# Performance work log

Hardware: AMD Instinct MI355X
Metric: run time of the kernel (lower is better)

## Reference

```python
import jax, jax.numpy as jnp
import numpy as np

HID, HEADS, NL, WIN = 512, 4, 2, 5
DH = HID // HEADS
SLOPE = 0.2
EPS = 1e-5
B, L = 16, 1024
NEG_INF = -1e30


def _layer_norm(x, g, b):
    m = jnp.mean(x, axis=-1, keepdims=True)
    v = jnp.mean(jnp.square(x - m), axis=-1, keepdims=True)
    return (x - m) * jax.lax.rsqrt(v + EPS) * g + b


def _build_masks(attention_mask, last_starts, seq_len):
    # node layout: [g, h_1..h_T, l], total N = seq_len + 2
    bsz = attention_mask.shape[0]
    N = seq_len + 2
    pos = jnp.arange(N)
    last = last_starts[:, None, None]  # (B,1,1)
    global_mask = jnp.ones((bsz, 1, N), jnp.float32)
    # local node: g, itself, and tokens of the last utterance (node idx last+1 .. seq_len)
    local_mask = ((pos == 0) | (pos == N - 1) | ((pos >= last + 1) & (pos <= seq_len))).astype(jnp.float32)  # (B,1,N)
    # token nodes: global node + window of neighboring tokens
    ii = jnp.arange(seq_len)[:, None]          # query token index
    jj = jnp.arange(N)[None, :]                # key node index
    t = jj - 1                                 # token index of key node (valid in [0, seq_len))
    win = (t >= 0) & (t < seq_len) & (jnp.abs(ii - t) <= WIN)
    base = (jj == 0) | win                     # (L,N)
    # tokens at/after last utterance start also attend to the local node
    to_local = (jnp.arange(seq_len)[None, :, None] >= last_starts[:, None, None]) & (jj[None] == N - 1)  # (B,L,N)
    token_mask = (base[None] | to_local).astype(jnp.float32)
    # padding: key tokens masked by attention_mask; g and l always visible; padded queries fully masked
    ones_col = jnp.ones((bsz, seq_len, 1), jnp.float32)
    pad = jnp.concatenate([ones_col, jnp.broadcast_to(attention_mask[:, None, :], (bsz, seq_len, seq_len)), ones_col], axis=-1)
    token_mask = token_mask * pad * attention_mask[:, :, None]
    return global_mask, local_mask, token_mask


def _gat(q, kv, W, a, mask):
    # W: (hid, hid) as torch Linear weight (out,in); a: (H, 2*DH)
    bsz, Lq, _ = q.shape
    N = kv.shape[1]
    Q = (q @ W.T).reshape(bsz, Lq, HEADS, DH)
    K = (kv @ W.T).reshape(bsz, N, HEADS, DH)
    V = K  # key==value tensor in this module, same projection
    # additive score decomposes: (a . [Q||K]) = Q.a_q + K.a_k
    sq = jnp.einsum('bqhd,hd->bhq', Q, a[:, :DH])
    sk = jnp.einsum('bkhd,hd->bhk', K, a[:, DH:])
    s = sq[:, :, :, None] + sk[:, :, None, :]           # (B,H,Lq,N)
    s = jnp.where(s >= 0, s, SLOPE * s)                 # LeakyReLU
    s = jnp.where(mask[:, None, :, :] > 0, s, NEG_INF)
    w = jax.nn.softmax(s, axis=-1)
    w = jnp.where(jnp.isnan(w), 0.0, w)
    out = jnp.einsum('bhqk,bkhd->bqhd', w, V)
    return out.reshape(bsz, Lq, HID)


def setup_inputs() -> dict:
    key = jax.random.key(0)
    ks = jax.random.split(key, 10)
    scale = 1.0 / np.sqrt(HID)
    return {
        'global_embedding': jax.random.normal(ks[0], (B, HID), jnp.float32),
        'token_embeddings': jax.random.normal(ks[1], (B, L, HID), jnp.float32),
        'local_embedding': jax.random.normal(ks[2], (B, HID), jnp.float32),
        'attention_mask': jnp.ones((B, L), jnp.float32),
        'last_utterance_starts': jax.random.randint(ks[3], (B,), 0, 512, jnp.int32),
        'gat_W': jax.random.normal(ks[4], (NL, HID, HID), jnp.float32) * scale,
        'gat_a': jax.random.normal(ks[5], (NL, HEADS, 2 * DH), jnp.float32) * scale,
        'ln_gamma': jnp.ones((NL, HID), jnp.float32),
        'ln_beta': jnp.zeros((NL, HID), jnp.float32),
        'ffn_w1': jax.random.normal(ks[6], (3, HID, 4 * HID), jnp.float32) * scale,
        'ffn_b1': jnp.zeros((3, 4 * HID), jnp.float32),
        'ffn_w2': jax.random.normal(ks[7], (3, 4 * HID, HID), jnp.float32) * (1.0 / np.sqrt(4 * HID)),
        'ffn_b2': jnp.zeros((3, HID), jnp.float32),
        'out_ln_gamma': jnp.ones((3, HID), jnp.float32),
        'out_ln_beta': jnp.zeros((3, HID), jnp.float32),
    }


def reference(global_embedding, token_embeddings, local_embedding, attention_mask,
              last_utterance_starts, gat_W, gat_a, ln_gamma, ln_beta,
              ffn_w1, ffn_b1, ffn_w2, ffn_b2, out_ln_gamma, out_ln_beta):
    bsz, seq_len, _ = token_embeddings.shape
    gm, lm, tm = _build_masks(attention_mask, last_utterance_starts, seq_len)
    g = global_embedding[:, None, :]
    h = token_embeddings
    l = local_embedding[:, None, :]
    nodes = jnp.concatenate([g, h, l], axis=1)
    for k in range(NL):
        g_new = jax.nn.elu(_gat(g, nodes, gat_W[k], gat_a[k], gm))
        h_new = jax.nn.elu(_gat(h, nodes, gat_W[k], gat_a[k], tm))
        l_new = jax.nn.elu(_gat(l, nodes, gat_W[k], gat_a[k], lm))
        g = _layer_norm(g + g_new, ln_gamma[k], ln_beta[k])
        h = _layer_norm(h + h_new, ln_gamma[k], ln_beta[k])
        l = _layer_norm(l + l_new, ln_gamma[k], ln_beta[k])
        nodes = jnp.concatenate([g, h, l], axis=1)
    def ffn(x, i):
        hmid = jax.nn.gelu(x @ ffn_w1[i] + ffn_b1[i], approximate=False)
        return hmid @ ffn_w2[i] + ffn_b2[i]
    g = g + ffn(g, 0)
    h = h + ffn(h, 1)
    l = l + ffn(l, 2)
    updated_global = _layer_norm(g[:, 0], out_ln_gamma[0], out_ln_beta[0])
    updated_tokens = _layer_norm(h, out_ln_gamma[1], out_ln_beta[1])
    updated_local = _layer_norm(l[:, 0], out_ln_gamma[2], out_ln_beta[2])
    return updated_global, updated_tokens, updated_local
```

## Files before the change

### kernel.cpp

```cpp
#include <hip/hip_runtime.h>
#include <stdint.h>
#include <math.h>

#define HIDN 512
#define NHEAD 4
#define DHEAD 128
#define BATCH 16
#define SEQ 1024
#define NNODE 1026
#define MROWS (BATCH * NNODE)
#define MPAD 16512
#define MTOK (BATCH * SEQ)
#define FFD 2048
#define JCH 114

typedef short bf16x8 __attribute__((ext_vector_type(8)));
typedef float f32x4 __attribute__((ext_vector_type(4)));

__device__ __forceinline__ float bf2f(ushort u) {
    union { uint32_t i; float f; } v; v.i = ((uint32_t)u) << 16; return v.f;
}
__device__ __forceinline__ ushort f2bf(float f) {
    uint32_t x = __float_as_uint(f);
    return (ushort)((x + 0x7fffu + ((x >> 16) & 1u)) >> 16);
}
__device__ __forceinline__ float gelu(float v) {
    float z = v * 0.70710678118654752f;
    float az = fabsf(z);
    float t = __builtin_amdgcn_rcpf(1.f + 0.3275911f * az);
    float y = ((((1.061405429f * t - 1.453152027f) * t + 1.421413741f) * t
                - 0.284496736f) * t + 0.254829592f) * t;
    float e = __expf(-az * az);
    float erfv = 1.f - y * e;
    erfv = (z >= 0.f) ? erfv : -erfv;
    return 0.5f * v * (1.f + erfv);
}
__device__ __forceinline__ int cswz(int row, int col) {
    return row * 128 + ((((col >> 2) ^ (row & 7)) & 31) << 2) + (col & 3);
}

__global__ __launch_bounds__(256) void k_build_nodes(
    const float* __restrict__ g, const float* __restrict__ tok,
    const float* __restrict__ l, ushort* __restrict__ nb)
{
    int idx = blockIdx.x * 256 + threadIdx.x;
    int r = idx >> 9, c = idx & 511;
    float u = 0.f;
    if (r < MROWS) {
        int b = r / NNODE;
        int n = r - b * NNODE;
        if (n == 0)            u = g[b * HIDN + c];
        else if (n <= SEQ)     u = tok[((size_t)b * SEQ + (n - 1)) * HIDN + c];
        else                   u = l[b * HIDN + c];
    }
    nb[idx] = f2bf(u);
}

__global__ __launch_bounds__(256) void k_cvt(
    const float* __restrict__ in, ushort* __restrict__ out, int n)
{
    int idx = blockIdx.x * 256 + threadIdx.x;
    if (idx < n) out[idx] = f2bf(in[idx]);
}

__global__ __launch_bounds__(256) void k_transpose(
    const float* __restrict__ in, ushort* __restrict__ out, int R, int C)
{
    __shared__ float t[32][33];
    int x = blockIdx.x * 32 + threadIdx.x;
    int y0 = blockIdx.y * 32;
    for (int dy = threadIdx.y; dy < 32; dy += 8)
        t[dy][threadIdx.x] = in[(size_t)(y0 + dy) * C + x];
    __syncthreads();
    int ox = y0 + threadIdx.x;
    int oy0 = blockIdx.x * 32;
    for (int dy = threadIdx.y; dy < 32; dy += 8)
        out[(size_t)(oy0 + dy) * R + ox] = f2bf(t[threadIdx.x][dy]);
}

#define BM 128
#define BN 128
#define BK 64

__global__ __launch_bounds__(256) void k_gemm_bt(
    const ushort* __restrict__ A, const ushort* __restrict__ Bt,
    float* __restrict__ Cf, ushort* __restrict__ Cb,
    const float* __restrict__ bias,
    int N, int K, int ldb, int mode, int amap, int mguard, int first)
{
    __shared__ ushort smem[2 * (BM * BK + BN * BK)];
    int tid = threadIdx.x;
    int lane = tid & 63;
    int wave = tid >> 6;
    int wm = wave >> 1, wn = wave & 1;

    int GX = gridDim.x;
    int nwg = GX * gridDim.y;
    int bid = blockIdx.y * GX + blockIdx.x;
    int q = nwg >> 3, r = nwg & 7;
    int xcd = bid & 7, pos = bid >> 3;
    int cbase = (xcd < r) ? xcd * (q + 1) : r * (q + 1) + (xcd - r) * q;
    int wk = cbase + pos;
    int m0 = (wk / GX) * BM;
    int n0 = (wk % GX) * BN;

    f32x4 acc[4][4];
#pragma unroll
    for (int i = 0; i < 4; ++i)
#pragma unroll
        for (int j = 0; j < 4; ++j) acc[i][j] = (f32x4){0.f, 0.f, 0.f, 0.f};

    int lr = lane >> 3;
    int gco = ((lane & 7) ^ lr) * 8;

    const ushort* pA[4];
    const ushort* pB[4];
#pragma unroll
    for (int u = 0; u < 4; ++u) {
        int qq = wave * 4 + u;
        int rr8 = qq * 8 + lr;
        int grA = m0 + rr8;
        if (amap) grA = grA + 2 * (grA >> 10) + 1;
        pA[u] = A + (size_t)grA * K + gco;
        int grB = n0 + rr8;
        pB[u] = Bt + (size_t)grB * ldb + gco;
    }

    auto stage = [&](int buf) {
        ushort* sA = smem + buf * (BM * BK + BN * BK);
        ushort* sB = sA + BM * BK;
#pragma unroll
        for (int u = 0; u < 4; ++u) {
            int qq = wave * 4 + u;
            __builtin_amdgcn_global_load_lds(
                (const __attribute__((address_space(1))) void*)pA[u],
                (__attribute__((address_space(3))) void*)&sA[qq * 512], 16, 0, 0);
            __builtin_amdgcn_global_load_lds(
                (const __attribute__((address_space(1))) void*)pB[u],
                (__attribute__((address_space(3))) void*)&sB[qq * 512], 16, 0, 0);
            pA[u] += BK;
            pB[u] += BK;
        }
    };

    const int nk = K / BK;
    stage(0);
    __syncthreads();

    int rr = lane & 7;
    int rhi = (lane & 15) >> 3;
    for (int t = 0; t < nk; ++t) {
        if (t + 1 < nk) stage((t + 1) & 1);

        const ushort* sAr = smem + (t & 1) * (BM * BK + BN * BK);
        const ushort* sBr = sAr + BM * BK;
#pragma unroll
        for (int kk = 0; kk < BK; kk += 32) {
            int c4 = (kk >> 3) + (lane >> 4);
            int swz = rr * 64 + ((c4 ^ rr) << 3);
            bf16x8 af[4], bfr[4];
#pragma unroll
            for (int i = 0; i < 4; ++i)
                af[i] = *reinterpret_cast<const bf16x8*>(&sAr[(wm * 8 + i * 2 + rhi) * 512 + swz]);
#pragma unroll
            for (int j = 0; j < 4; ++j)
                bfr[j] = *reinterpret_cast<const bf16x8*>(&sBr[(wn * 8 + j * 2 + rhi) * 512 + swz]);
#pragma unroll
            for (int i = 0; i < 4; ++i)
#pragma unroll
                for (int j = 0; j < 4; ++j)
                    acc[i][j] = __builtin_amdgcn_mfma_f32_16x16x32_bf16(af[i], bfr[j], acc[i][j], 0, 0, 0);
        }
        asm volatile("s_waitcnt vmcnt(0)" ::: "memory");
        __builtin_amdgcn_s_barrier();
    }
    __syncthreads();

    float* sC = (float*)smem;
    int rb = (lane >> 4) * 4;
    int cb = lane & 15;
    int lrow = tid >> 2;
    int lcol = (tid & 3) << 5;
#pragma unroll
    for (int pass = 0; pass < 2; ++pass) {
        if (wm == pass) {
#pragma unroll
            for (int i = 0; i < 4; ++i)
#pragma unroll
                for (int j = 0; j < 4; ++j)
#pragma unroll
                    for (int rg = 0; rg < 4; ++rg)
                        sC[cswz(i * 16 + rb + rg, wn * 64 + j * 16 + cb)] = acc[i][j][rg];
        }
        __syncthreads();
        int gm = m0 + pass * 64 + lrow;
        if (gm < mguard) {
            int gn0 = n0 + lcol;
            float v[32];
#pragma unroll
            for (int e4 = 0; e4 < 8; ++e4) {
                float4 t = *(const float4*)&sC[cswz(lrow, lcol + e4 * 4)];
                v[e4 * 4 + 0] = t.x; v[e4 * 4 + 1] = t.y;
                v[e4 * 4 + 2] = t.z; v[e4 * 4 + 3] = t.w;
            }
            if (mode == 1 || mode == 3) {
                if (mode == 3) {
                    const float* a1 = bias + (gn0 >> 7) * 256 + (gn0 & 127);
                    const float* a2 = a1 + 128;
                    float s1 = 0.f, s2 = 0.f;
#pragma unroll
                    for (int j = 0; j < 32; ++j) {
                        s1 += v[j] * a1[j];
                        s2 += v[j] * a2[j];
                    }
                    s1 += __shfl_xor(s1, 1); s1 += __shfl_xor(s1, 2);
                    s2 += __shfl_xor(s2, 1); s2 += __shfl_xor(s2, 2);
                    if ((tid & 3) == 0) {
                        Cf[gm * 4 + (gn0 >> 7)] = s1;
                        Cf[(size_t)MPAD * 4 + gm * 4 + (gn0 >> 7)] = s2;
                    }
                }
                uint4* dst = (uint4*)(Cb + (size_t)gm * N + gn0);
#pragma unroll
                for (int q2 = 0; q2 < 4; ++q2) {
                    float s[8];
#pragma unroll
                    for (int t = 0; t < 8; ++t) {
                        float x = v[q2 * 8 + t];
                        s[t] = (mode == 1) ? gelu(x + bias[gn0 + q2 * 8 + t]) : x;
                    }
                    uint4 w;
                    w.x = (uint32_t)f2bf(s[0]) | ((uint32_t)f2bf(s[1]) << 16);
                    w.y = (uint32_t)f2bf(s[2]) | ((uint32_t)f2bf(s[3]) << 16);
                    w.z = (uint32_t)f2bf(s[4]) | ((uint32_t)f2bf(s[5]) << 16);
                    w.w = (uint32_t)f2bf(s[6]) | ((uint32_t)f2bf(s[7]) << 16);
                    dst[q2] = w;
                }
            } else {
                float4* dst = (float4*)(Cf + (size_t)gm * N + gn0);
#pragma unroll
                for (int e4 = 0; e4 < 8; ++e4) {
                    float4 t;
                    t.x = v[e4 * 4 + 0]; t.y = v[e4 * 4 + 1];
                    t.z = v[e4 * 4 + 2]; t.w = v[e4 * 4 + 3];
                    if (!first) {
                        float4 o = dst[e4];
                        t.x += o.x; t.y += o.y; t.z += o.z; t.w += o.w;
                    }
                    dst[e4] = t;
                }
            }
        }
        __syncthreads();
    }
}

#define QK 64

template<int NB>
__global__ __launch_bounds__(512) void k_g256(
    const ushort* __restrict__ A, const ushort* __restrict__ Bt,
    float* __restrict__ Cf, ushort* __restrict__ Cb,
    const float* __restrict__ bias,
    int N, int K, int mode, int amap)
{
    extern __shared__ ushort smem[];
    constexpr int FJ   = NB / 64;
    constexpr int BCH  = NB / 64;
    constexpr int BUFU = 16384 + NB * 64;
    constexpr int CW   = NB / 4;
    constexpr int CMSK = CW - 1;

    int tid = threadIdx.x;
    int lane = tid & 63;
    int wave = tid >> 6;
    int wr = wave >> 2;
    int wc = wave & 3;

    int GX = gridDim.x;
    int nwg = GX * gridDim.y;
    int bid = blockIdx.y * GX + blockIdx.x;
    int cpx = nwg >> 3;
    int wk = (bid & 7) * cpx + (bid >> 3);
    int m0 = (wk / GX) * 256;
    int n0 = (wk % GX) * NB;

    f32x4 acc[8][FJ];
#pragma unroll
    for (int i = 0; i < 8; ++i)
#pragma unroll
        for (int j = 0; j < FJ; ++j) acc[i][j] = (f32x4){0.f, 0.f, 0.f, 0.f};

    int lr = lane >> 3;
    int gco = ((lane & 7) ^ lr) * 8;

    const ushort* pA[4];
    const ushort* pB[BCH];
#pragma unroll
    for (int u = 0; u < 4; ++u) {
        int q = wave * 4 + u;
        int grA = m0 + q * 8 + lr;
        if (amap) grA = grA + 2 * (grA >> 10) + 1;
        pA[u] = A + (size_t)grA * K + gco;
    }
#pragma unroll
    for (int u = 0; u < BCH; ++u) {
        int q = wave * BCH + u;
        int grB = n0 + q * 8 + lr;
        pB[u] = Bt + (size_t)grB * K + gco;
    }

    auto stage = [&](int buf) {
        ushort* sA = smem + buf * BUFU;
        ushort* sB = sA + 16384;
#pragma unroll
        for (int u = 0; u < 4; ++u) {
            int q = wave * 4 + u;
            __builtin_amdgcn_global_load_lds(
                (const __attribute__((address_space(1))) void*)pA[u],
                (__attribute__((address_space(3))) void*)&sA[q * 512], 16, 0, 0);
            pA[u] += QK;
        }
#pragma unroll
        for (int u = 0; u < BCH; ++u) {
            int q = wave * BCH + u;
            __builtin_amdgcn_global_load_lds(
                (const __attribute__((address_space(1))) void*)pB[u],
                (__attribute__((address_space(3))) void*)&sB[q * 512], 16, 0, 0);
            pB[u] += QK;
        }
    };

    const int nk = K / QK;
    stage(0);
    __syncthreads();

    int rr = lane & 7;
    int rhi = (lane & 15) >> 3;
    for (int t = 0; t < nk; ++t) {
        if (t + 1 < nk) stage((t + 1) & 1);

        const ushort* sAr = smem + (t & 1) * BUFU;
        const ushort* sBr = sAr + 16384;
#pragma unroll
        for (int kk = 0; kk < 2; ++kk) {
            int c4 = kk * 4 + (lane >> 4);
            int swz = rr * 64 + ((c4 ^ rr) << 3);
#pragma unroll
            for (int fi0 = 0; fi0 < 8; fi0 += 4) {
                bf16x8 af[4];
#pragma unroll
                for (int i = 0; i < 4; ++i) {
                    int qA = wr * 16 + (fi0 + i) * 2 + rhi;
                    af[i] = *reinterpret_cast<const bf16x8*>(&sAr[qA * 512 + swz]);
                }
#pragma unroll
                for (int fj0 = 0; fj0 < FJ; fj0 += 2) {
                    bf16x8 bfr[2];
#pragma unroll
                    for (int j = 0; j < 2; ++j) {
                        int qB = wc * (NB / 32) + (fj0 + j) * 2 + rhi;
                        bfr[j] = *reinterpret_cast<const bf16x8*>(&sBr[qB * 512 + swz]);
                    }
#pragma unroll
                    for (int i = 0; i < 4; ++i)
#pragma unroll
                        for (int j = 0; j < 2; ++j)
                            acc[fi0 + i][fj0 + j] = __builtin_amdgcn_mfma_f32_16x16x32_bf16(
                                af[i], bfr[j], acc[fi0 + i][fj0 + j], 0, 0, 0);
                }
            }
        }
        __syncthreads();
    }

    float* sC = (float*)smem;
    int rb = (lane >> 4) * 4;
    int cb = lane & 15;
    int lrow = tid >> 2;
    int lcol = (tid & 3) * CW;
#pragma unroll
    for (int pass = 0; pass < 2; ++pass) {
        if (wr == pass) {
#pragma unroll
            for (int fi = 0; fi < 8; ++fi)
#pragma unroll
                for (int fj = 0; fj < FJ; ++fj)
#pragma unroll
                    for (int rg = 0; rg < 4; ++rg) {
                        int row = fi * 16 + rb + rg;
                        int col = wc * CW + fj * 16 + cb;
                        sC[row * NB + ((((col >> 2) ^ (row & 7)) & CMSK) << 2) + (col & 3)] =
                            acc[fi][fj][rg];
                    }
        }
        __syncthreads();
        int gm = m0 + pass * 128 + lrow;
        if (mode == 1) {
            uint4* dst = (uint4*)(Cb + (size_t)gm * N + n0 + lcol);
#pragma unroll
            for (int g = 0; g < CW / 8; ++g) {
                int col = lcol + g * 8;
                float4 a = *(const float4*)&sC[lrow * NB + ((((col >> 2) ^ (lrow & 7)) & CMSK) << 2)];
                float4 b = *(const float4*)&sC[lrow * NB + (((((col + 4) >> 2) ^ (lrow & 7)) & CMSK) << 2)];
                const float* bp = bias + n0 + col;
                float s0 = gelu(a.x + bp[0]), s1 = gelu(a.y + bp[1]);
                float s2 = gelu(a.z + bp[2]), s3 = gelu(a.w + bp[3]);
                float s4 = gelu(b.x + bp[4]), s5 = gelu(b.y + bp[5]);
                float s6 = gelu(b.z + bp[6]), s7 = gelu(b.w + bp[7]);
                uint4 w;
                w.x = (uint32_t)f2bf(s0) | ((uint32_t)f2bf(s1) << 16);
                w.y = (uint32_t)f2bf(s2) | ((uint32_t)f2bf(s3) << 16);
                w.z = (uint32_t)f2bf(s4) | ((uint32_t)f2bf(s5) << 16);
                w.w = (uint32_t)f2bf(s6) | ((uint32_t)f2bf(s7) << 16);
                dst[g] = w;
            }
        } else {
            float4* dst = (float4*)(Cf + (size_t)gm * N + n0 + lcol);
#pragma unroll
            for (int e4 = 0; e4 < CW / 4; ++e4) {
                int col = lcol + e4 * 4;
                float4 tv = *(const float4*)&sC[lrow * NB + ((((col >> 2) ^ (lrow & 7)) & CMSK) << 2)];
                dst[e4] = tv;
            }
        }
        __syncthreads();
    }
}

__global__ __launch_bounds__(256) void k_attn_token(
    const ushort* __restrict__ P, const float* __restrict__ sq, const float* __restrict__ sk,
    const float* __restrict__ am, const int* __restrict__ last,
    const float* __restrict__ gam, const float* __restrict__ bet,
    ushort* __restrict__ nb)
{
    int wid = blockIdx.x * 4 + (threadIdx.x >> 6);
    int tokid = ((wid & 7) << 11) | (wid >> 3);
    int b = tokid >> 10, i = tokid & 1023;
    int lane = threadIdx.x & 63;
    int hh = lane >> 4;
    int base = b * NNODE;
    int qrow = base + 1 + i;

    int kr[13];
    int val[13];
    int rowok = am[b * SEQ + i] > 0.f ? 1 : 0;
    kr[0] = base; val[0] = rowok;
#pragma unroll
    for (int s = 0; s < 11; ++s) {
        int t = i - 5 + s;
        int inb = (t >= 0) && (t <= SEQ - 1);
        int tt = inb ? t : 0;
        int v = inb && rowok && (am[b * SEQ + tt] > 0.f);
        kr[1 + s] = base + 1 + tt;
        val[1 + s] = v;
    }
    kr[12] = base + SEQ + 1;
    val[12] = (rowok && (i >= last[b])) ? 1 : 0;

    float sqv = sq[qrow * 4 + hh];
    float sc[13];
    float mx = -1e30f;
#pragma unroll
    for (int t = 0; t < 13; ++t) {
        float s = 0.f;
        if (val[t]) {
            s = sqv + sk[kr[t] * 4 + hh];
            s = s >= 0.f ? s : 0.2f * s;
            mx = fmaxf(mx, s);
        }
        sc[t] = s;
    }
    float den = 0.f;
#pragma unroll
    for (int t = 0; t < 13; ++t) {
        float ev = 0.f;
        if (val[t]) ev = expf(sc[t] - mx);
        sc[t] = ev; den += ev;
    }
    float inv = (den > 1e-30f && den < 1e30f) ? 1.f / den : 0.f;

    int o0 = lane * 8;
    float accv[8] = {0.f, 0.f, 0.f, 0.f, 0.f, 0.f, 0.f, 0.f};
#pragma unroll
    for (int t = 0; t < 13; ++t) {
        if (val[t]) {
            float wgt = sc[t] * inv;
            const ushort* pv = P + (size_t)kr[t] * HIDN + o0;
#pragma unroll
            for (int d = 0; d < 8; ++d) accv[d] += wgt * bf2f(pv[d]);
        }
    }

    ushort* nrow = nb + (size_t)qrow * HIDN + o0;
    float x[8], s1 = 0.f, s2 = 0.f;
#pragma unroll
    for (int d = 0; d < 8; ++d) {
        float v = accv[d];
        v = v > 0.f ? v : expf(v) - 1.f;
        v += bf2f(nrow[d]);
        x[d] = v; s1 += v; s2 += v * v;
    }
#pragma unroll
    for (int off = 32; off; off >>= 1) { s1 += __shfl_xor(s1, off); s2 += __shfl_xor(s2, off); }
    float mean = s1 * (1.f / 512.f);
    float var = s2 * (1.f / 512.f) - mean * mean; var = fmaxf(var, 0.f);
    float rn = rsqrtf(var + 1e-5f);
#pragma unroll
    for (int d = 0; d < 8; ++d) {
        float y = (x[d] - mean) * rn * gam[o0 + d] + bet[o0 + d];
        nrow[d] = f2bf(y);
    }
}

__global__ __launch_bounds__(256) void k_glsm(
    const float* __restrict__ sq, const float* __restrict__ sk,
    const int* __restrict__ last,
    float* __restrict__ ebuf, float* __restrict__ einv)
{
    __shared__ float red[1024];
    int rw = blockIdx.x, b = rw >> 1, isl = rw & 1;
    int base = b * NNODE;
    int qrow = base + (isl ? (SEQ + 1) : 0);
    int lastb = last[b];
    int tid = threadIdx.x;

    float sqh[4];
#pragma unroll
    for (int h = 0; h < 4; ++h) sqh[h] = sq[qrow * 4 + h];

    float mx[4] = {-1e30f, -1e30f, -1e30f, -1e30f};
    for (int j = tid; j < NNODE; j += 256) {
        bool ok = !isl || (j == 0 || j == SEQ + 1 || (j >= lastb + 1 && j <= SEQ));
        if (ok) {
#pragma unroll
            for (int h = 0; h < 4; ++h) {
                float s = sqh[h] + sk[(base + j) * 4 + h];
                s = s >= 0.f ? s : 0.2f * s;
                mx[h] = fmaxf(mx[h], s);
            }
        }
    }
#pragma unroll
    for (int h = 0; h < 4; ++h) red[tid * 4 + h] = mx[h];
    __syncthreads();
    for (int s = 128; s; s >>= 1) {
        if (tid < s) {
#pragma unroll
            for (int h = 0; h < 4; ++h)
                red[tid * 4 + h] = fmaxf(red[tid * 4 + h], red[(tid + s) * 4 + h]);
        }
        __syncthreads();
    }
#pragma unroll
    for (int h = 0; h < 4; ++h) mx[h] = red[h];
    __syncthreads();

    float sm[4] = {0.f, 0.f, 0.f, 0.f};
    for (int j = tid; j < NNODE; j += 256) {
        bool ok = !isl || (j == 0 || j == SEQ + 1 || (j >= lastb + 1 && j <= SEQ));
#pragma unroll
        for (int h = 0; h < 4; ++h) {
            float v = 0.f;
            if (ok) {
                float s = sqh[h] + sk[(base + j) * 4 + h];
                s = s >= 0.f ? s : 0.2f * s;
                v = expf(s - mx[h]);
            }
            ebuf[((size_t)rw * NNODE + j) * 4 + h] = v;
            sm[h] += v;
        }
    }
#pragma unroll
    for (int h = 0; h < 4; ++h) red[tid * 4 + h] = sm[h];
    __syncthreads();
    for (int s = 128; s; s >>= 1) {
        if (tid < s) {
#pragma unroll
            for (int h = 0; h < 4; ++h) red[tid * 4 + h] += red[(tid + s) * 4 + h];
        }
        __syncthreads();
    }
    if (tid < 4) {
        float den = red[tid];
        einv[rw * 4 + tid] = (den > 1e-30f && den < 1e30f) ? 1.f / den : 0.f;
    }
}

__global__ __launch_bounds__(256) void k_glpv(
    const ushort* __restrict__ P, const float* __restrict__ ebuf,
    float* __restrict__ pout2)
{
    __shared__ float es[JCH * 4];
    int p = blockIdx.x, rw = blockIdx.y;
    int b = rw >> 1;
    int base = b * NNODE;
    int tid = threadIdx.x;
    for (int t = tid; t < JCH * 4; t += 256)
        es[t] = ebuf[((size_t)rw * NNODE + p * JCH) * 4 + t];
    __syncthreads();
    int o0 = tid, o1 = tid + 256;
    int h0 = o0 >> 7, h1 = o1 >> 7;
    const ushort* Pb = P + (size_t)(base + p * JCH) * HIDN;
    float a0 = 0.f, a1 = 0.f;
    for (int j = 0; j < JCH; ++j) {
        const ushort* pr = Pb + (size_t)j * HIDN;
        a0 += es[j * 4 + h0] * bf2f(pr[o0]);
        a1 += es[j * 4 + h1] * bf2f(pr[o1]);
    }
    float* o = pout2 + ((size_t)rw * 9 + p) * HIDN;
    o[o0] = a0;
    o[o1] = a1;
}

__global__ __launch_bounds__(256) void k_glred(
    const float* __restrict__ pout2, const float* __restrict__ einv,
    const float* __restrict__ gam, const float* __restrict__ bet,
    ushort* __restrict__ nb)
{
    __shared__ float red[512];
    int rw = blockIdx.x, b = rw >> 1, isl = rw & 1;
    size_t qrow = (size_t)b * NNODE + (isl ? SEQ + 1 : 0);
    int tid = threadIdx.x;
    float xv[2], s1 = 0.f, s2 = 0.f;
#pragma unroll
    for (int u = 0; u < 2; ++u) {
        int o = tid + u * 256;
        int h = o >> 7;
        float acc = 0.f;
#pragma unroll
        for (int p = 0; p < 9; ++p)
            acc += pout2[((size_t)rw * 9 + p) * HIDN + o];
        acc *= einv[rw * 4 + h];
        float v = acc > 0.f ? acc : expf(acc) - 1.f;
        v += bf2f(nb[qrow * HIDN + o]);
        xv[u] = v; s1 += v; s2 += v * v;
    }
    red[tid] = s1;
    __syncthreads();
    for (int s = 128; s; s >>= 1) { if (tid < s) red[tid] += red[tid + s]; __syncthreads(); }
    float mean = red[0] * (1.f / 512.f);
    __syncthreads();
    red[tid] = s2;
    __syncthreads();
    for (int s = 128; s; s >>= 1) { if (tid < s) red[tid] += red[tid + s]; __syncthreads(); }
    float var = red[0] * (1.f / 512.f) - mean * mean; var = fmaxf(var, 0.f);
    float rn = rsqrtf(var + 1e-5f);
#pragma unroll
    for (int u = 0; u < 2; ++u) {
        int o = tid + u * 256;
        float y = (xv[u] - mean) * rn * gam[o] + bet[o];
        nb[qrow * HIDN + o] = f2bf(y);
    }
}

__global__ __launch_bounds__(256) void k_fgl1(
    const ushort* __restrict__ nb, const float* __restrict__ w1,
    float* __restrict__ pmid)
{
    __shared__ float xs[64];
    int p = blockIdx.x, rw = blockIdx.y;
    int b = rw >> 1, isl = rw & 1;
    int idx = isl ? 2 : 0;
    size_t nrow = (size_t)b * NNODE + (isl ? SEQ + 1 : 0);
    int tid = threadIdx.x;
    if (tid < 64) xs[tid] = bf2f(nb[nrow * HIDN + p * 64 + tid]);
    __syncthreads();
    const float* W1 = w1 + (size_t)idx * HIDN * FFD + (size_t)p * 64 * FFD;
    float acc[8] = {0.f, 0.f, 0.f, 0.f, 0.f, 0.f, 0.f, 0.f};
    for (int ii = 0; ii < 64; ++ii) {
        float xv = xs[ii];
        const float* wrow = W1 + (size_t)ii * FFD + tid;
#pragma unroll
        for (int u = 0; u < 8; ++u) acc[u] += xv * wrow[u * 256];
    }
    float* o = pmid + ((size_t)rw * 8 + p) * FFD + tid;
#pragma unroll
    for (int u = 0; u < 8; ++u) o[u * 256] = acc[u];
}

__global__ __launch_bounds__(256) void k_fgl2(
    const float* __restrict__ pmid, const float* __restrict__ b1,
    float* __restrict__ mid)
{
    int g = blockIdx.x * 256 + threadIdx.x;
    int e4 = g * 4;
    int rw = e4 >> 11;
    int m = e4 & 2047;
    int isl = rw & 1;
    int idx = isl ? 2 : 0;
#pragma unroll
    for (int d = 0; d < 4; ++d) {
        float s = 0.f;
#pragma unroll
        for (int p = 0; p < 8; ++p)
            s += pmid[((size_t)rw * 8 + p) * FFD + m + d];
        s += b1[idx * FFD + m + d];
        mid[(size_t)rw * FFD + m + d] = gelu(s);
    }
}

__global__ __launch_bounds__(256) void k_fgl3(
    const float* __restrict__ mid, const float* __restrict__ w2,
    float* __restrict__ pout)
{
    __shared__ float ms[256];
    int p = blockIdx.x, rw = blockIdx.y;
    int isl = rw & 1;
    int idx = isl ? 2 : 0;
    int tid = threadIdx.x;
    ms[tid] = mid[(size_t)rw * FFD + p * 256 + tid];
    __syncthreads();
    const float* W2 = w2 + (size_t)idx * FFD * HIDN + (size_t)p * 256 * HIDN;
    float a0 = 0.f, a1 = 0.f;
    for (int mm = 0; mm < 256; ++mm) {
        float mv = ms[mm];
        const float* wrow = W2 + (size_t)mm * HIDN + tid;
        a0 += mv * wrow[0];
        a1 += mv * wrow[256];
    }
    float* o = pout + ((size_t)rw * 8 + p) * HIDN + tid;
    o[0] = a0;
    o[256] = a1;
}

__global__ __launch_bounds__(256) void k_fgl4(
    const float* __restrict__ pout, const float* __restrict__ b2,
    const ushort* __restrict__ nb,
    const float* __restrict__ og, const float* __restrict__ obt,
    float* __restrict__ out)
{
    __shared__ float red[512];
    int rw = blockIdx.x;
    int b = rw >> 1, isl = rw & 1;
    int idx = isl ? 2 : 0;
    size_t nrow = (size_t)b * NNODE + (isl ? SEQ + 1 : 0);
    int tid = threadIdx.x;
    float xv[2], s1 = 0.f, s2 = 0.f;
#pragma unroll
    for (int u = 0; u < 2; ++u) {
        int o = tid + u * 256;
        float s = 0.f;
#pragma unroll
        for (int p = 0; p < 8; ++p)
            s += pout[((size_t)rw * 8 + p) * HIDN + o];
        s += b2[idx * HIDN + o] + bf2f(nb[nrow * HIDN + o]);
        xv[u] = s; s1 += s; s2 += s * s;
    }
    red[tid] = s1;
    __syncthreads();
    for (int s = 128; s; s >>= 1) { if (tid < s) red[tid] += red[tid + s]; __syncthreads(); }
    float mean = red[0] * (1.f / 512.f);
    __syncthreads();
    red[tid] = s2;
    __syncthreads();
    for (int s = 128; s; s >>= 1) { if (tid < s) red[tid] += red[tid + s]; __syncthreads(); }
    float var = red[0] * (1.f / 512.f) - mean * mean; var = fmaxf(var, 0.f);
    float rn = rsqrtf(var + 1e-5f);
    size_t obase = isl ? ((size_t)8192 + (size_t)MTOK * HIDN + (size_t)b * HIDN)
                       : ((size_t)b * HIDN);
#pragma unroll
    for (int u = 0; u < 2; ++u) {
        int o = tid + u * 256;
        out[obase + o] = (xv[u] - mean) * rn * og[idx * HIDN + o] + obt[idx * HIDN + o];
    }
}

__global__ __launch_bounds__(64) void k_ln_final(
    float* __restrict__ Pt, const ushort* __restrict__ nb,
    const float* __restrict__ b2,
    const float* __restrict__ gam, const float* __restrict__ bet)
{
    int r = blockIdx.x, lane = threadIdx.x;
    int nrow = r + 2 * (r >> 10) + 1;
    int o0 = lane * 8;
    float* x = Pt + (size_t)r * HIDN + o0;
    const ushort* res = nb + (size_t)nrow * HIDN + o0;
    float v[8], s1 = 0.f, s2 = 0.f;
#pragma unroll
    for (int d = 0; d < 8; ++d) {
        float t = x[d] + b2[o0 + d] + bf2f(res[d]);
        v[d] = t; s1 += t; s2 += t * t;
    }
#pragma unroll
    for (int off = 32; off; off >>= 1) { s1 += __shfl_xor(s1, off); s2 += __shfl_xor(s2, off); }
    float mean = s1 * (1.f / 512.f);
    float var = s2 * (1.f / 512.f) - mean * mean; var = fmaxf(var, 0.f);
    float rn = rsqrtf(var + 1e-5f);
#pragma unroll
    for (int d = 0; d < 8; ++d)
        x[d] = (v[d] - mean) * rn * gam[o0 + d] + bet[o0 + d];
}

extern "C" void kernel_launch(void* const* d_in, const int* in_sizes, int n_in,
                              void* d_out, int out_size, void* d_ws, size_t ws_size,
                              hipStream_t stream)
{
    (void)in_sizes; (void)n_in; (void)out_size; (void)ws_size;
    const float* g_emb   = (const float*)d_in[0];
    const float* tok_emb = (const float*)d_in[1];
    const float* l_emb   = (const float*)d_in[2];
    const float* am      = (const float*)d_in[3];
    const int*   last    = (const int*)d_in[4];
    const float* gat_W   = (const float*)d_in[5];
    const float* gat_a   = (const float*)d_in[6];
    const float* ln_g    = (const float*)d_in[7];
    const float* ln_b    = (const float*)d_in[8];
    const float* ffn_w1  = (const float*)d_in[9];
    const float* ffn_b1  = (const float*)d_in[10];
    const float* ffn_w2  = (const float*)d_in[11];
    const float* ffn_b2  = (const float*)d_in[12];
    const float* oln_g   = (const float*)d_in[13];
    const float* oln_b   = (const float*)d_in[14];
    float* out = (float*)d_out;

    char* w = (char*)d_ws;
    ushort* nodes_b = (ushort*)w; w += (size_t)MPAD * HIDN * 2;
    char*   scratch = w;          w += (size_t)8 * 1024 * 1024;
    ushort* w1t     = (ushort*)w; w += (size_t)FFD * HIDN * 2;
    ushort* w2t     = (ushort*)w; w += (size_t)FFD * HIDN * 2;
    ushort* gatWb   = (ushort*)w; w += (size_t)2 * HIDN * HIDN * 2;
    float*  sqb     = (float*)w;  w += (size_t)MPAD * 4 * 4;
    float*  skb     = (float*)w;  w += (size_t)MPAD * 4 * 4;
    ushort* Hmid    = (ushort*)w; w += (size_t)MTOK * FFD * 2;

    float* pmid = (float*)scratch;
    float* mid  = pmid + (size_t)32 * 8 * FFD;
    float* pout = mid + (size_t)32 * FFD;
    float* ebuf  = (float*)(scratch + (size_t)3 * 1024 * 1024);
    float* einv  = ebuf + (size_t)32 * NNODE * 4;
    float* pout2 = einv + 128;

    ushort* P = (ushort*)out;
    float* Pt = out + 8192;

    k_build_nodes<<<MPAD * HIDN / 256, 256, 0, stream>>>(g_emb, tok_emb, l_emb, nodes_b);
    k_cvt<<<(2 * HIDN * HIDN) / 256, 256, 0, stream>>>(gat_W, gatWb, 2 * HIDN * HIDN);
    k_transpose<<<dim3(FFD / 32, HIDN / 32), dim3(32, 8), 0, stream>>>(ffn_w1 + (size_t)HIDN * FFD, w1t, HIDN, FFD);
    k_transpose<<<dim3(HIDN / 32, FFD / 32), dim3(32, 8), 0, stream>>>(ffn_w2 + (size_t)FFD * HIDN, w2t, FFD, HIDN);

    for (int k = 0; k < 2; ++k) {
        k_gemm_bt<<<dim3(HIDN / BN, MPAD / BM), 256, 0, stream>>>(
            nodes_b, gatWb + (size_t)k * HIDN * HIDN, sqb, P,
            gat_a + k * NHEAD * 2 * DHEAD,
            HIDN, HIDN, HIDN, 3, 0, MROWS, 1);
        k_attn_token<<<MTOK / 4, 256, 0, stream>>>(P, sqb, skb, am, last,
                                                   ln_g + k * HIDN, ln_b + k * HIDN, nodes_b);
        k_glsm<<<32, 256, 0, stream>>>(sqb, skb, last, ebuf, einv);
        k_glpv<<<dim3(9, 32), 256, 0, stream>>>(P, ebuf, pout2);
        k_glred<<<32, 256, 0, stream>>>(pout2, einv, ln_g + k * HIDN, ln_b + k * HIDN, nodes_b);
    }

    k_fgl1<<<dim3(8, 32), 256, 0, stream>>>(nodes_b, ffn_w1, pmid);
    k_fgl2<<<64, 256, 0, stream>>>(pmid, ffn_b1, mid);
    k_fgl3<<<dim3(8, 32), 256, 0, stream>>>(mid, ffn_w2, pout);
    k_fgl4<<<32, 256, 0, stream>>>(pout, ffn_b2, nodes_b, oln_g, oln_b, out);

    k_g256<256><<<dim3(FFD / 256, MTOK / 256), 512, 131072, stream>>>(
        nodes_b, w1t, nullptr, Hmid, ffn_b1 + FFD, FFD, HIDN, 1, 1);
    k_g256<128><<<dim3(HIDN / 128, MTOK / 256), 512, 98304, stream>>>(
        Hmid, w2t, Pt, nullptr, nullptr, HIDN, FFD, 0, 0);
    k_ln_final<<<MTOK, 64, 0, stream>>>(Pt, nodes_b, ffn_b2 + HIDN, oln_g + HIDN, oln_b + HIDN);
}
```

Before: 477.6 us.

## Fuse global/local node attention softmax, PV and layernorm into one kernel

New measurement: 692.4 us. +45.0%, slower.

```diff
diff --git a/kernel.cpp b/kernel.cpp
--- a/kernel.cpp
+++ b/kernel.cpp
@@ -12,7 +12,6 @@
 #define MPAD 16512
 #define MTOK (BATCH * SEQ)
 #define FFD 2048
-#define JCH 114
 
 typedef short bf16x8 __attribute__((ext_vector_type(8)));
 typedef float f32x4 __attribute__((ext_vector_type(4)));
@@ -513,144 +512,116 @@
     }
 }
 
-__global__ __launch_bounds__(256) void k_glsm(
-    const float* __restrict__ sq, const float* __restrict__ sk,
-    const int* __restrict__ last,
-    float* __restrict__ ebuf, float* __restrict__ einv)
-{
-    __shared__ float red[1024];
+__global__ __launch_bounds__(1024) void k_glatt(
+    const ushort* __restrict__ P, const float* __restrict__ sq,
+    const float* __restrict__ sk, const int* __restrict__ last,
+    const float* __restrict__ gam, const float* __restrict__ bet,
+    ushort* __restrict__ nb)
+{
+    __shared__ float es[NNODE * 4];
+    __shared__ float red[64];
+    __shared__ float xv2[512];
     int rw = blockIdx.x, b = rw >> 1, isl = rw & 1;
     int base = b * NNODE;
-    int qrow = base + (isl ? (SEQ + 1) : 0);
+    size_t qrow = (size_t)base + (isl ? (SEQ + 1) : 0);
     int lastb = last[b];
     int tid = threadIdx.x;
+    int lane = tid & 63, wave = tid >> 6;
 
     float sqh[4];
 #pragma unroll
     for (int h = 0; h < 4; ++h) sqh[h] = sq[qrow * 4 + h];
 
     float mx[4] = {-1e30f, -1e30f, -1e30f, -1e30f};
-    for (int j = tid; j < NNODE; j += 256) {
+    for (int j = tid; j < NNODE; j += 1024) {
         bool ok = !isl || (j == 0 || j == SEQ + 1 || (j >= lastb + 1 && j <= SEQ));
-        if (ok) {
-#pragma unroll
-            for (int h = 0; h < 4; ++h) {
-                float s = sqh[h] + sk[(base + j) * 4 + h];
+#pragma unroll
+        for (int h = 0; h < 4; ++h) {
+            float s = -1e30f;
+            if (ok) {
+                s = sqh[h] + sk[(base + j) * 4 + h];
                 s = s >= 0.f ? s : 0.2f * s;
                 mx[h] = fmaxf(mx[h], s);
             }
-        }
-    }
-#pragma unroll
-    for (int h = 0; h < 4; ++h) red[tid * 4 + h] = mx[h];
-    __syncthreads();
-    for (int s = 128; s; s >>= 1) {
-        if (tid < s) {
-#pragma unroll
-            for (int h = 0; h < 4; ++h)
-                red[tid * 4 + h] = fmaxf(red[tid * 4 + h], red[(tid + s) * 4 + h]);
-        }
-        __syncthreads();
-    }
-#pragma unroll
-    for (int h = 0; h < 4; ++h) mx[h] = red[h];
+            es[j * 4 + h] = s;
+        }
+    }
+#pragma unroll
+    for (int off = 32; off; off >>= 1)
+#pragma unroll
+        for (int h = 0; h < 4; ++h) mx[h] = fmaxf(mx[h], __shfl_xor(mx[h], off));
+    if (lane == 0) {
+#pragma unroll
+        for (int h = 0; h < 4; ++h) red[wave * 4 + h] = mx[h];
+    }
+    __syncthreads();
+#pragma unroll
+    for (int h = 0; h < 4; ++h) {
+        float m = -1e30f;
+        for (int w2 = 0; w2 < 16; ++w2) m = fmaxf(m, red[w2 * 4 + h]);
+        mx[h] = m;
+    }
     __syncthreads();
 
     float sm[4] = {0.f, 0.f, 0.f, 0.f};
-    for (int j = tid; j < NNODE; j += 256) {
-        bool ok = !isl || (j == 0 || j == SEQ + 1 || (j >= lastb + 1 && j <= SEQ));
+    for (int j = tid; j < NNODE; j += 1024) {
 #pragma unroll
         for (int h = 0; h < 4; ++h) {
-            float v = 0.f;
-            if (ok) {
-                float s = sqh[h] + sk[(base + j) * 4 + h];
-                s = s >= 0.f ? s : 0.2f * s;
-                v = expf(s - mx[h]);
-            }
-            ebuf[((size_t)rw * NNODE + j) * 4 + h] = v;
-            sm[h] += v;
-        }
-    }
-#pragma unroll
-    for (int h = 0; h < 4; ++h) red[tid * 4 + h] = sm[h];
-    __syncthreads();
-    for (int s = 128; s; s >>= 1) {
-        if (tid < s) {
-#pragma unroll
-            for (int h = 0; h < 4; ++h) red[tid * 4 + h] += red[(tid + s) * 4 + h];
-        }
-        __syncthreads();
-    }
-    if (tid < 4) {
-        float den = red[tid];
-        einv[rw * 4 + tid] = (den > 1e-30f && den < 1e30f) ? 1.f / den : 0.f;
-    }
-}
-
-__global__ __launch_bounds__(256) void k_glpv(
-    const ushort* __restrict__ P, const float* __restrict__ ebuf,
-    float* __restrict__ pout2)
-{
-    __shared__ float es[JCH * 4];
-    int p = blockIdx.x, rw = blockIdx.y;
-    int b = rw >> 1;
-    int base = b * NNODE;
-    int tid = threadIdx.x;
-    for (int t = tid; t < JCH * 4; t += 256)
-        es[t] = ebuf[((size_t)rw * NNODE + p * JCH) * 4 + t];
-    __syncthreads();
-    int o0 = tid, o1 = tid + 256;
-    int h0 = o0 >> 7, h1 = o1 >> 7;
-    const ushort* Pb = P + (size_t)(base + p * JCH) * HIDN;
-    float a0 = 0.f, a1 = 0.f;
-    for (int j = 0; j < JCH; ++j) {
-        const ushort* pr = Pb + (size_t)j * HIDN;
-        a0 += es[j * 4 + h0] * bf2f(pr[o0]);
-        a1 += es[j * 4 + h1] * bf2f(pr[o1]);
-    }
-    float* o = pout2 + ((size_t)rw * 9 + p) * HIDN;
-    o[o0] = a0;
-    o[o1] = a1;
-}
-
-__global__ __launch_bounds__(256) void k_glred(
-    const float* __restrict__ pout2, const float* __restrict__ einv,
-    const float* __restrict__ gam, const float* __restrict__ bet,
-    ushort* __restrict__ nb)
-{
-    __shared__ float red[512];
-    int rw = blockIdx.x, b = rw >> 1, isl = rw & 1;
-    size_t qrow = (size_t)b * NNODE + (isl ? SEQ + 1 : 0);
-    int tid = threadIdx.x;
-    float xv[2], s1 = 0.f, s2 = 0.f;
-#pragma unroll
-    for (int u = 0; u < 2; ++u) {
-        int o = tid + u * 256;
-        int h = o >> 7;
-        float acc = 0.f;
-#pragma unroll
-        for (int p = 0; p < 9; ++p)
-            acc += pout2[((size_t)rw * 9 + p) * HIDN + o];
-        acc *= einv[rw * 4 + h];
-        float v = acc > 0.f ? acc : expf(acc) - 1.f;
-        v += bf2f(nb[qrow * HIDN + o]);
-        xv[u] = v; s1 += v; s2 += v * v;
-    }
-    red[tid] = s1;
-    __syncthreads();
-    for (int s = 128; s; s >>= 1) { if (tid < s) red[tid] += red[tid + s]; __syncthreads(); }
-    float mean = red[0] * (1.f / 512.f);
-    __syncthreads();
-    red[tid] = s2;
-    __syncthreads();
-    for (int s = 128; s; s >>= 1) { if (tid < s) red[tid] += red[tid + s]; __syncthreads(); }
-    float var = red[0] * (1.f / 512.f) - mean * mean; var = fmaxf(var, 0.f);
+            float e = expf(es[j * 4 + h] - mx[h]);
+            es[j * 4 + h] = e;
+            sm[h] += e;
+        }
+    }
+#pragma unroll
+    for (int off = 32; off; off >>= 1)
+#pragma unroll
+        for (int h = 0; h < 4; ++h) sm[h] += __shfl_xor(sm[h], off);
+    if (lane == 0) {
+#pragma unroll
+        for (int h = 0; h < 4; ++h) red[wave * 4 + h] = sm[h];
+    }
+    __syncthreads();
+    float inv4[4];
+#pragma unroll
+    for (int h = 0; h < 4; ++h) {
+        float den = 0.f;
+        for (int w2 = 0; w2 < 16; ++w2) den += red[w2 * 4 + h];
+        inv4[h] = (den > 1e-30f && den < 1e30f) ? 1.f / den : 0.f;
+    }
+
+    int d = tid & 511, half = tid >> 9;
+    int h = d >> 7;
+    float acc = 0.f;
+    for (int j0 = half * 4; j0 < NNODE; j0 += 8) {
+#pragma unroll
+        for (int u = 0; u < 4; ++u) {
+            int j = j0 + u;
+            if (j < NNODE)
+                acc += es[j * 4 + h] * bf2f(P[(size_t)(base + j) * HIDN + d]);
+        }
+    }
+    if (half == 1) xv2[d] = acc;
+    __syncthreads();
+
+    float v = 0.f;
+    if (half == 0) {
+        float a = (acc + xv2[d]) * inv4[h];
+        v = a > 0.f ? a : expf(a) - 1.f;
+        v += bf2f(nb[qrow * HIDN + d]);
+    }
+    float s1 = v, s2 = v * v;
+#pragma unroll
+    for (int off = 32; off; off >>= 1) { s1 += __shfl_xor(s1, off); s2 += __shfl_xor(s2, off); }
+    if (lane == 0) { red[wave] = s1; red[16 + wave] = s2; }
+    __syncthreads();
+    float t1 = 0.f, t2 = 0.f;
+    for (int w2 = 0; w2 < 16; ++w2) { t1 += red[w2]; t2 += red[16 + w2]; }
+    float mean = t1 * (1.f / 512.f);
+    float var = t2 * (1.f / 512.f) - mean * mean; var = fmaxf(var, 0.f);
     float rn = rsqrtf(var + 1e-5f);
-#pragma unroll
-    for (int u = 0; u < 2; ++u) {
-        int o = tid + u * 256;
-        float y = (xv[u] - mean) * rn * gam[o] + bet[o];
-        nb[qrow * HIDN + o] = f2bf(y);
+    if (half == 0) {
+        float y = (v - mean) * rn * gam[d] + bet[d];
+        nb[qrow * HIDN + d] = f2bf(y);
     }
 }
 
@@ -827,9 +798,6 @@
     float* pmid = (float*)scratch;
     float* mid  = pmid + (size_t)32 * 8 * FFD;
     float* pout = mid + (size_t)32 * FFD;
-    float* ebuf  = (float*)(scratch + (size_t)3 * 1024 * 1024);
-    float* einv  = ebuf + (size_t)32 * NNODE * 4;
-    float* pout2 = einv + 128;
 
     ushort* P = (ushort*)out;
     float* Pt = out + 8192;
@@ -846,9 +814,8 @@
             HIDN, HIDN, HIDN, 3, 0, MROWS, 1);
         k_attn_token<<<MTOK / 4, 256, 0, stream>>>(P, sqb, skb, am, last,
                                                    ln_g + k * HIDN, ln_b + k * HIDN, nodes_b);
-        k_glsm<<<32, 256, 0, stream>>>(sqb, skb, last, ebuf, einv);
-        k_glpv<<<dim3(9, 32), 256, 0, stream>>>(P, ebuf, pout2);
-        k_glred<<<32, 256, 0, stream>>>(pout2, einv, ln_g + k * HIDN, ln_b + k * HIDN, nodes_b);
+        k_glatt<<<32, 1024, 0, stream>>>(P, sqb, skb, last,
+                                         ln_g + k * HIDN, ln_b + k * HIDN, nodes_b);
     }
 
     k_fgl1<<<dim3(8, 32), 256, 0, stream>>>(nodes_b, ffn_w1, pmid);
```
